# Performance work log

Hardware: AMD Instinct MI355X
Metric: run time of the kernel (lower is better)

## Reference

```python
import jax, jax.numpy as jnp
import numpy as np

N_NODES = 10000
N_EDGES = 320000
D_IN = 256
D_OUT = 256
NEG_SLOPE = 0.2


def setup_inputs() -> dict:
    key = jax.random.key(0)
    ks = jax.random.split(key, 8)
    feature = jax.random.normal(ks[0], (N_NODES, D_IN), dtype=jnp.float32)
    src = jax.random.randint(ks[1], (N_EDGES,), 0, N_NODES, dtype=jnp.int32)
    dst = jax.random.randint(ks[2], (N_EDGES,), 0, N_NODES, dtype=jnp.int32)
    # Xavier-ish scaled weights
    s = 1.0 / np.sqrt(D_IN)
    W_s = jax.random.normal(ks[3], (D_OUT, D_IN), dtype=jnp.float32) * s
    W_t = jax.random.normal(ks[4], (D_OUT, D_IN), dtype=jnp.float32) * s
    W_attn = jax.random.normal(ks[5], (1, D_OUT), dtype=jnp.float32) * (1.0 / np.sqrt(D_OUT))
    W_fc = jax.random.normal(ks[6], (D_OUT, D_IN), dtype=jnp.float32) * s
    b_fc = jnp.zeros((D_OUT,), dtype=jnp.float32)
    return {"feature": feature, "src": src, "dst": dst,
            "W_s": W_s, "W_t": W_t, "W_attn": W_attn,
            "W_fc": W_fc, "b_fc": b_fc}


def reference(feature, src, dst, W_s, W_t, W_attn, W_fc, b_fc):
    n = feature.shape[0]
    # Project at node level, then gather (same math as projecting gathered feats).
    proj_s = feature @ W_s.T          # [N, D_OUT]
    proj_t = feature @ W_t.T          # [N, D_OUT]
    # Edge attention logits: attn(LeakyReLU(h_dst + h_src))
    z = proj_s[src] + proj_t[dst]     # [E, D_OUT]
    z = jnp.where(z >= 0, z, NEG_SLOPE * z)
    e = (z @ W_attn.T)[:, 0]          # [E]
    # edge_softmax with norm_by='src': softmax over outgoing edges of each src node
    m = jax.ops.segment_max(e, src, num_segments=n)          # [N]
    m = jnp.where(jnp.isfinite(m), m, 0.0)                   # guard empty segments
    e_exp = jnp.exp(e - m[src])                               # [E]
    denom = jax.ops.segment_sum(e_exp, src, num_segments=n)  # [N]
    alpha = e_exp / denom[src]                                # [E]
    # message = src feature * alpha; reduce = sum at dst
    msg = feature[src] * alpha[:, None]                       # [E, D_IN]
    agg = jax.ops.segment_sum(msg, dst, num_segments=n)       # [N, D_IN]
    # final linear
    return agg @ W_fc.T + b_fc
```

## Files before the change

### kernel.cpp

```cpp
#include <hip/hip_runtime.h>
#include <math.h>

#define N_NODES 10000
#define N_EDGES 320000
#define D 256
#define NEG_SLOPE 0.2f
#define BCAP 96
#define BLOCK 256
#define NF4 (N_NODES * D / 4)
#define NW4 (256 * 256 / 4)
#define NTILE_M 157
#define NTILES (NTILE_M * 12)
#define FILL_BLOCKS ((N_EDGES + BLOCK - 1) / BLOCK)
#define CPAD 66

typedef unsigned short ushortT;
typedef __attribute__((ext_vector_type(8))) short bf16x8;
typedef __attribute__((ext_vector_type(4))) float f32x4;

__device__ __forceinline__ unsigned short f2bf(float f) {
  unsigned int u = __float_as_uint(f);
  u += 0x7FFFu + ((u >> 16) & 1u);
  return (unsigned short)(u >> 16);
}
__device__ __forceinline__ float bf2f(unsigned short u) {
  return __uint_as_float((unsigned int)u << 16);
}

typedef const __attribute__((address_space(1))) unsigned int* gas_ptr;
typedef __attribute__((address_space(3))) unsigned int* las_ptr;
__device__ __forceinline__ void gload16(const void* g, void* l) {
  __builtin_amdgcn_global_load_lds((gas_ptr)g, (las_ptr)l, 16, 0, 0);
}

__global__ void prep_kernel(const float* __restrict__ feat,
                            const float* __restrict__ Ws,
                            const float* __restrict__ Wt,
                            const float* __restrict__ Wfc,
                            ushortT* __restrict__ featb,
                            ushortT* __restrict__ Wcat,
                            int* __restrict__ cnt,
                            float* __restrict__ denom) {
  const int g = blockIdx.x * blockDim.x + threadIdx.x;
  if (g < NF4) {
    float4 v = ((const float4*)feat)[g];
    ushort4 u;
    u.x = f2bf(v.x); u.y = f2bf(v.y); u.z = f2bf(v.z); u.w = f2bf(v.w);
    ((ushort4*)featb)[g] = u;
    return;
  }
  const int gi = g - NF4;
  if (gi < 3 * NW4) {
    const float* W = (gi < NW4) ? Ws : ((gi < 2 * NW4) ? Wt : Wfc);
    const int off = gi - ((gi < NW4) ? 0 : ((gi < 2 * NW4) ? NW4 : 2 * NW4));
    float4 v = ((const float4*)W)[off];
    ushort4 u;
    u.x = f2bf(v.x); u.y = f2bf(v.y); u.z = f2bf(v.z); u.w = f2bf(v.w);
    ((ushort4*)Wcat)[gi] = u;
    return;
  }
  const int gn = gi - 3 * NW4;
  if (gn < N_NODES) {
    cnt[gn] = 0;
    denom[gn] = 0.f;
  }
}

__global__ __launch_bounds__(256, 2) void proj_fill_kernel(
    const ushortT* __restrict__ featb,
    const ushortT* __restrict__ Wcat,
    const int* __restrict__ src, const int* __restrict__ dst,
    int* __restrict__ cnt, int* __restrict__ src_b,
    ushortT* __restrict__ ps, ushortT* __restrict__ pt,
    ushortT* __restrict__ fcp) {
  __shared__ ushortT Als[64][D];
  __shared__ ushortT Bls[64][D];
  __shared__ ushortT Cls[64][CPAD];

  if (blockIdx.x < FILL_BLOCKS) {
    const int i = blockIdx.x * BLOCK + threadIdx.x;
    if (i < N_EDGES) {
      const int dn = dst[i];
      const int slot = atomicAdd(&cnt[dn], 1);
      if (slot < BCAP) src_b[dn * BCAP + slot] = src[i];
    }
    return;
  }
  const int p = blockIdx.x - FILL_BLOCKS;
  const int m0 = (p / 12) * 64;
  const int by = p % 12;
  ushortT* outp = (by < 4) ? ps : ((by < 8) ? pt : fcp);
  const int col0 = (by & 3) * 64;
  const int n0 = by * 64;

  const int tid = threadIdx.x;
  const int wave = tid >> 6;
  const int lane = tid & 63;
  const int quad = lane >> 4;
  const int l16 = lane & 15;

  const int m_base_t = (wave & 1) * 32;
  const int wn = wave >> 1;

  {
    const int rl = lane >> 5;
    const int cph = lane & 31;
#pragma unroll
    for (int c = 0; c < 8; ++c) {
      const int r = wave * 16 + c * 2 + rl;
      const int clog = cph ^ (r & 7);
      gload16(featb + (size_t)(m0 + r) * D + clog * 8, &Als[wave * 16 + c * 2][0]);
      gload16(Wcat + (size_t)(n0 + r) * D + clog * 8, &Bls[wave * 16 + c * 2][0]);
    }
  }
  __syncthreads();

  f32x4 acc[2][2];
#pragma unroll
  for (int i = 0; i < 2; ++i)
#pragma unroll
    for (int j = 0; j < 2; ++j) acc[i][j] = (f32x4){0.f, 0.f, 0.f, 0.f};

  const int ar0 = m_base_t + l16;
  const int br0 = wn * 32 + l16;
  const int xa = ar0 & 7;
  const int xb = br0 & 7;
#pragma unroll
  for (int kk = 0; kk < 8; ++kk) {
    const int j = kk * 4 + quad;
    const int ea = (j ^ xa) * 8;
    const int eb = (j ^ xb) * 8;
    bf16x8 a0 = *(const bf16x8*)&Als[ar0][ea];
    bf16x8 a1 = *(const bf16x8*)&Als[ar0 + 16][ea];
    bf16x8 b0 = *(const bf16x8*)&Bls[br0][eb];
    bf16x8 b1 = *(const bf16x8*)&Bls[br0 + 16][eb];
    acc[0][0] = __builtin_amdgcn_mfma_f32_16x16x32_bf16(a0, b0, acc[0][0], 0, 0, 0);
    acc[0][1] = __builtin_amdgcn_mfma_f32_16x16x32_bf16(a0, b1, acc[0][1], 0, 0, 0);
    acc[1][0] = __builtin_amdgcn_mfma_f32_16x16x32_bf16(a1, b0, acc[1][0], 0, 0, 0);
    acc[1][1] = __builtin_amdgcn_mfma_f32_16x16x32_bf16(a1, b1, acc[1][1], 0, 0, 0);
  }

#pragma unroll
  for (int mi = 0; mi < 2; ++mi)
#pragma unroll
    for (int r = 0; r < 4; ++r) {
      const int row = m_base_t + mi * 16 + quad * 4 + r;
#pragma unroll
      for (int ni = 0; ni < 2; ++ni)
        Cls[row][wn * 32 + ni * 16 + l16] = f2bf(acc[mi][ni][r]);
    }
  __syncthreads();
#pragma unroll
  for (int it = 0; it < 2; ++it) {
    const int idx = tid + it * 256;
    const int row = idx >> 3;
    const int cc = (idx & 7) * 8;
    const int grow = m0 + row;
    if (grow < N_NODES)
      *(bf16x8*)(outp + (size_t)grow * D + col0 + cc) = *(const bf16x8*)&Cls[row][cc];
  }
}

__global__ __launch_bounds__(256) void logit_bucket_kernel(
    const ushortT* __restrict__ ps,
    const ushortT* __restrict__ pt,
    const int* __restrict__ cnt,
    const int* __restrict__ src_b,
    const float* __restrict__ Wattn,
    float* __restrict__ expv_b,
    float* __restrict__ denom) {
  const int wave = threadIdx.x >> 6;
  const int n = blockIdx.x * 4 + wave;
  if (n >= N_NODES) return;
  const int cn = min(cnt[n], BCAP);
  if (cn == 0) return;
  const int lane = threadIdx.x & 63;
  const int half = lane >> 5;
  const int l32 = lane & 31;
  const int base = n * BCAP;

  bf16x8 bu = *(const bf16x8*)(pt + (size_t)n * D + l32 * 8);
  float b[8], w[8];
  const float4 w0 = *(const float4*)(Wattn + l32 * 8);
  const float4 w1 = *(const float4*)(Wattn + l32 * 8 + 4);
  w[0] = w0.x; w[1] = w0.y; w[2] = w0.z; w[3] = w0.w;
  w[4] = w1.x; w[5] = w1.y; w[6] = w1.z; w[7] = w1.w;
#pragma unroll
  for (int i = 0; i < 8; ++i) b[i] = bf2f((unsigned short)bu[i]);

  int j = half;
  for (; j + 6 < cn; j += 8) {
    const int s0 = src_b[base + j];
    const int s1 = src_b[base + j + 2];
    const int s2 = src_b[base + j + 4];
    const int s3 = src_b[base + j + 6];
    bf16x8 au0 = *(const bf16x8*)(ps + (size_t)s0 * D + l32 * 8);
    bf16x8 au1 = *(const bf16x8*)(ps + (size_t)s1 * D + l32 * 8);
    bf16x8 au2 = *(const bf16x8*)(ps + (size_t)s2 * D + l32 * 8);
    bf16x8 au3 = *(const bf16x8*)(ps + (size_t)s3 * D + l32 * 8);
    float sum0 = 0.f, sum1 = 0.f, sum2 = 0.f, sum3 = 0.f;
#pragma unroll
    for (int i = 0; i < 8; ++i) {
      float z0 = bf2f((unsigned short)au0[i]) + b[i];
      float z1 = bf2f((unsigned short)au1[i]) + b[i];
      float z2 = bf2f((unsigned short)au2[i]) + b[i];
      float z3 = bf2f((unsigned short)au3[i]) + b[i];
      z0 = fmaxf(z0, NEG_SLOPE * z0);
      z1 = fmaxf(z1, NEG_SLOPE * z1);
      z2 = fmaxf(z2, NEG_SLOPE * z2);
      z3 = fmaxf(z3, NEG_SLOPE * z3);
      sum0 = fmaf(w[i], z0, sum0);
      sum1 = fmaf(w[i], z1, sum1);
      sum2 = fmaf(w[i], z2, sum2);
      sum3 = fmaf(w[i], z3, sum3);
    }
#pragma unroll
    for (int off = 16; off > 0; off >>= 1) {
      sum0 += __shfl_down(sum0, off, 32);
      sum1 += __shfl_down(sum1, off, 32);
      sum2 += __shfl_down(sum2, off, 32);
      sum3 += __shfl_down(sum3, off, 32);
    }
    if (l32 == 0) {
      float ex0 = __expf(sum0), ex1 = __expf(sum1);
      float ex2 = __expf(sum2), ex3 = __expf(sum3);
      expv_b[base + j] = ex0;
      expv_b[base + j + 2] = ex1;
      expv_b[base + j + 4] = ex2;
      expv_b[base + j + 6] = ex3;
      atomicAdd(&denom[s0], ex0);
      atomicAdd(&denom[s1], ex1);
      atomicAdd(&denom[s2], ex2);
      atomicAdd(&denom[s3], ex3);
    }
  }
  for (; j < cn; j += 2) {
    const int s = src_b[base + j];
    bf16x8 au = *(const bf16x8*)(ps + (size_t)s * D + l32 * 8);
    float sum = 0.f;
#pragma unroll
    for (int i = 0; i < 8; ++i) {
      float z = bf2f((unsigned short)au[i]) + b[i];
      z = fmaxf(z, NEG_SLOPE * z);
      sum = fmaf(w[i], z, sum);
    }
#pragma unroll
    for (int off = 16; off > 0; off >>= 1) sum += __shfl_down(sum, off, 32);
    if (l32 == 0) {
      float ex = __expf(sum);
      expv_b[base + j] = ex;
      atomicAdd(&denom[s], ex);
    }
  }
}

__global__ __launch_bounds__(256) void gather_agg_kernel(
    const ushortT* __restrict__ fcp,
    const int* __restrict__ cnt,
    const int* __restrict__ src_b,
    const float* __restrict__ expv_b,
    const float* __restrict__ denom,
    const float* __restrict__ b_fc,
    float* __restrict__ out) {
  const int wave = threadIdx.x >> 6;
  const int n = blockIdx.x * 4 + wave;
  if (n >= N_NODES) return;
  const int lane = threadIdx.x & 63;
  const int half = lane >> 5;
  const int l32 = lane & 31;
  const int cn = min(cnt[n], BCAP);
  const int base = n * BCAP;

  float acc[8];
#pragma unroll
  for (int i = 0; i < 8; ++i) acc[i] = 0.f;

  int j = half;
  for (; j + 6 < cn; j += 8) {
    const int s0 = src_b[base + j];
    const int s1 = src_b[base + j + 2];
    const int s2 = src_b[base + j + 4];
    const int s3 = src_b[base + j + 6];
    const float a0 = expv_b[base + j] / denom[s0];
    const float a1 = expv_b[base + j + 2] / denom[s1];
    const float a2 = expv_b[base + j + 4] / denom[s2];
    const float a3 = expv_b[base + j + 6] / denom[s3];
    bf16x8 f0 = *(const bf16x8*)(fcp + (size_t)s0 * D + l32 * 8);
    bf16x8 f1 = *(const bf16x8*)(fcp + (size_t)s1 * D + l32 * 8);
    bf16x8 f2 = *(const bf16x8*)(fcp + (size_t)s2 * D + l32 * 8);
    bf16x8 f3 = *(const bf16x8*)(fcp + (size_t)s3 * D + l32 * 8);
#pragma unroll
    for (int i = 0; i < 8; ++i) {
      acc[i] = fmaf(a0, bf2f((unsigned short)f0[i]), acc[i]);
      acc[i] = fmaf(a1, bf2f((unsigned short)f1[i]), acc[i]);
      acc[i] = fmaf(a2, bf2f((unsigned short)f2[i]), acc[i]);
      acc[i] = fmaf(a3, bf2f((unsigned short)f3[i]), acc[i]);
    }
  }
  for (; j < cn; j += 2) {
    const int s = src_b[base + j];
    const float a = expv_b[base + j] / denom[s];
    bf16x8 fu = *(const bf16x8*)(fcp + (size_t)s * D + l32 * 8);
#pragma unroll
    for (int i = 0; i < 8; ++i)
      acc[i] = fmaf(a, bf2f((unsigned short)fu[i]), acc[i]);
  }
#pragma unroll
  for (int i = 0; i < 8; ++i) acc[i] += __shfl_xor(acc[i], 32);
  if (half == 0) {
    const float4 bf0 = *(const float4*)(b_fc + l32 * 8);
    const float4 bf1 = *(const float4*)(b_fc + l32 * 8 + 4);
    float4 o0 = make_float4(acc[0] + bf0.x, acc[1] + bf0.y, acc[2] + bf0.z, acc[3] + bf0.w);
    float4 o1 = make_float4(acc[4] + bf1.x, acc[5] + bf1.y, acc[6] + bf1.z, acc[7] + bf1.w);
    *(float4*)(out + (size_t)n * D + l32 * 8) = o0;
    *(float4*)(out + (size_t)n * D + l32 * 8 + 4) = o1;
  }
}

extern "C" void kernel_launch(void* const* d_in, const int* in_sizes, int n_in,
                              void* d_out, int out_size, void* d_ws, size_t ws_size,
                              hipStream_t stream) {
  const float* feat  = (const float*)d_in[0];
  const int*   src   = (const int*)d_in[1];
  const int*   dst   = (const int*)d_in[2];
  const float* Ws    = (const float*)d_in[3];
  const float* Wt    = (const float*)d_in[4];
  const float* Wattn = (const float*)d_in[5];
  const float* Wfc   = (const float*)d_in[6];
  const float* bfc   = (const float*)d_in[7];
  float* out = (float*)d_out;

  ushortT* ps    = (ushortT*)d_ws;
  ushortT* pt    = ps + (size_t)N_NODES * D;
  ushortT* fcp   = pt + (size_t)N_NODES * D;
  ushortT* featb = fcp + (size_t)N_NODES * D;
  ushortT* Wcat  = featb + (size_t)N_NODES * D;
  float* expv_b  = (float*)(Wcat + (size_t)768 * 256);
  float* denom   = expv_b + (size_t)N_NODES * BCAP;
  int*   cnt     = (int*)(denom + N_NODES);
  int*   src_b   = cnt + N_NODES;

  const int prep_items = NF4 + 3 * NW4 + N_NODES;
  const int nodeblocks = (N_NODES + 3) / 4;
  prep_kernel<<<(prep_items + BLOCK - 1) / BLOCK, BLOCK, 0, stream>>>(
      feat, Ws, Wt, Wfc, featb, Wcat, cnt, denom);
  proj_fill_kernel<<<FILL_BLOCKS + NTILES, BLOCK, 0, stream>>>(
      featb, Wcat, src, dst, cnt, src_b, ps, pt, fcp);
  logit_bucket_kernel<<<nodeblocks, BLOCK, 0, stream>>>(ps, pt, cnt, src_b, Wattn, expv_b, denom);
  gather_agg_kernel<<<nodeblocks, BLOCK, 0, stream>>>(fcp, cnt, src_b, expv_b, denom, bfc, out);
}
```

Before: 162.1 us.

## Load B tile into registers, vectorize edge index loads, use fast reciprocal

The projection GEMM now loads its weight fragments straight from global memory into registers instead of staging them in LDS. That removes the Bls buffer, and the occupancy hint rises from 2 to 3 blocks. The attention and aggregate kernels now have each half-wave handle four contiguous edge slots, read with int4/float4 vector loads and written with a float4 store, instead of strided scalar accesses. The exact division by denom is replaced with a v_rcp_f32 reciprocal times the value, trading a little precision for fewer instructions. The extra register arrays may raise register pressure against the higher occupancy target.

```diff
diff --git a/kernel.cpp b/kernel.cpp
--- a/kernel.cpp
+++ b/kernel.cpp
@@ -25,6 +25,11 @@
 }
 __device__ __forceinline__ float bf2f(unsigned short u) {
   return __uint_as_float((unsigned int)u << 16);
+}
+__device__ __forceinline__ float fastrcp(float x) {
+  float r;
+  asm volatile("v_rcp_f32 %0, %1" : "=v"(r) : "v"(x));
+  return r;
 }
 
 typedef const __attribute__((address_space(1))) unsigned int* gas_ptr;
@@ -66,7 +71,7 @@
   }
 }
 
-__global__ __launch_bounds__(256, 2) void proj_fill_kernel(
+__global__ __launch_bounds__(256, 3) void proj_fill_kernel(
     const ushortT* __restrict__ featb,
     const ushortT* __restrict__ Wcat,
     const int* __restrict__ src, const int* __restrict__ dst,
@@ -74,7 +79,6 @@
     ushortT* __restrict__ ps, ushortT* __restrict__ pt,
     ushortT* __restrict__ fcp) {
   __shared__ ushortT Als[64][D];
-  __shared__ ushortT Bls[64][D];
   __shared__ ushortT Cls[64][CPAD];
 
   if (blockIdx.x < FILL_BLOCKS) {
@@ -101,6 +105,14 @@
 
   const int m_base_t = (wave & 1) * 32;
   const int wn = wave >> 1;
+  const int br0 = wn * 32 + l16;
+
+  bf16x8 b0r[8], b1r[8];
+#pragma unroll
+  for (int kk = 0; kk < 8; ++kk) {
+    b0r[kk] = *(const bf16x8*)(Wcat + (size_t)(n0 + br0) * D + kk * 32 + quad * 8);
+    b1r[kk] = *(const bf16x8*)(Wcat + (size_t)(n0 + br0 + 16) * D + kk * 32 + quad * 8);
+  }
 
   {
     const int rl = lane >> 5;
@@ -110,7 +122,6 @@
       const int r = wave * 16 + c * 2 + rl;
       const int clog = cph ^ (r & 7);
       gload16(featb + (size_t)(m0 + r) * D + clog * 8, &Als[wave * 16 + c * 2][0]);
-      gload16(Wcat + (size_t)(n0 + r) * D + clog * 8, &Bls[wave * 16 + c * 2][0]);
     }
   }
   __syncthreads();
@@ -122,22 +133,16 @@
     for (int j = 0; j < 2; ++j) acc[i][j] = (f32x4){0.f, 0.f, 0.f, 0.f};
 
   const int ar0 = m_base_t + l16;
-  const int br0 = wn * 32 + l16;
   const int xa = ar0 & 7;
-  const int xb = br0 & 7;
 #pragma unroll
   for (int kk = 0; kk < 8; ++kk) {
-    const int j = kk * 4 + quad;
-    const int ea = (j ^ xa) * 8;
-    const int eb = (j ^ xb) * 8;
+    const int ea = ((kk * 4 + quad) ^ xa) * 8;
     bf16x8 a0 = *(const bf16x8*)&Als[ar0][ea];
     bf16x8 a1 = *(const bf16x8*)&Als[ar0 + 16][ea];
-    bf16x8 b0 = *(const bf16x8*)&Bls[br0][eb];
-    bf16x8 b1 = *(const bf16x8*)&Bls[br0 + 16][eb];
-    acc[0][0] = __builtin_amdgcn_mfma_f32_16x16x32_bf16(a0, b0, acc[0][0], 0, 0, 0);
-    acc[0][1] = __builtin_amdgcn_mfma_f32_16x16x32_bf16(a0, b1, acc[0][1], 0, 0, 0);
-    acc[1][0] = __builtin_amdgcn_mfma_f32_16x16x32_bf16(a1, b0, acc[1][0], 0, 0, 0);
-    acc[1][1] = __builtin_amdgcn_mfma_f32_16x16x32_bf16(a1, b1, acc[1][1], 0, 0, 0);
+    acc[0][0] = __builtin_amdgcn_mfma_f32_16x16x32_bf16(a0, b0r[kk], acc[0][0], 0, 0, 0);
+    acc[0][1] = __builtin_amdgcn_mfma_f32_16x16x32_bf16(a0, b1r[kk], acc[0][1], 0, 0, 0);
+    acc[1][0] = __builtin_amdgcn_mfma_f32_16x16x32_bf16(a1, b0r[kk], acc[1][0], 0, 0, 0);
+    acc[1][1] = __builtin_amdgcn_mfma_f32_16x16x32_bf16(a1, b1r[kk], acc[1][1], 0, 0, 0);
   }
 
 #pragma unroll
@@ -188,16 +193,13 @@
 #pragma unroll
   for (int i = 0; i < 8; ++i) b[i] = bf2f((unsigned short)bu[i]);
 
-  int j = half;
-  for (; j + 6 < cn; j += 8) {
-    const int s0 = src_b[base + j];
-    const int s1 = src_b[base + j + 2];
-    const int s2 = src_b[base + j + 4];
-    const int s3 = src_b[base + j + 6];
-    bf16x8 au0 = *(const bf16x8*)(ps + (size_t)s0 * D + l32 * 8);
-    bf16x8 au1 = *(const bf16x8*)(ps + (size_t)s1 * D + l32 * 8);
-    bf16x8 au2 = *(const bf16x8*)(ps + (size_t)s2 * D + l32 * 8);
-    bf16x8 au3 = *(const bf16x8*)(ps + (size_t)s3 * D + l32 * 8);
+  const int cn4 = cn & ~7;
+  for (int j = half * 4; j < cn4; j += 8) {
+    const int4 s4 = *(const int4*)(src_b + base + j);
+    bf16x8 au0 = *(const bf16x8*)(ps + (size_t)s4.x * D + l32 * 8);
+    bf16x8 au1 = *(const bf16x8*)(ps + (size_t)s4.y * D + l32 * 8);
+    bf16x8 au2 = *(const bf16x8*)(ps + (size_t)s4.z * D + l32 * 8);
+    bf16x8 au3 = *(const bf16x8*)(ps + (size_t)s4.w * D + l32 * 8);
     float sum0 = 0.f, sum1 = 0.f, sum2 = 0.f, sum3 = 0.f;
 #pragma unroll
     for (int i = 0; i < 8; ++i) {
@@ -224,17 +226,14 @@
     if (l32 == 0) {
       float ex0 = __expf(sum0), ex1 = __expf(sum1);
       float ex2 = __expf(sum2), ex3 = __expf(sum3);
-      expv_b[base + j] = ex0;
-      expv_b[base + j + 2] = ex1;
-      expv_b[base + j + 4] = ex2;
-      expv_b[base + j + 6] = ex3;
-      atomicAdd(&denom[s0], ex0);
-      atomicAdd(&denom[s1], ex1);
-      atomicAdd(&denom[s2], ex2);
-      atomicAdd(&denom[s3], ex3);
-    }
-  }
-  for (; j < cn; j += 2) {
+      *(float4*)(expv_b + base + j) = make_float4(ex0, ex1, ex2, ex3);
+      atomicAdd(&denom[s4.x], ex0);
+      atomicAdd(&denom[s4.y], ex1);
+      atomicAdd(&denom[s4.z], ex2);
+      atomicAdd(&denom[s4.w], ex3);
+    }
+  }
+  for (int j = cn4 + half; j < cn; j += 2) {
     const int s = src_b[base + j];
     bf16x8 au = *(const bf16x8*)(ps + (size_t)s * D + l32 * 8);
     float sum = 0.f;
@@ -275,20 +274,18 @@
 #pragma unroll
   for (int i = 0; i < 8; ++i) acc[i] = 0.f;
 
-  int j = half;
-  for (; j + 6 < cn; j += 8) {
-    const int s0 = src_b[base + j];
-    const int s1 = src_b[base + j + 2];
-    const int s2 = src_b[base + j + 4];
-    const int s3 = src_b[base + j + 6];
-    const float a0 = expv_b[base + j] / denom[s0];
-    const float a1 = expv_b[base + j + 2] / denom[s1];
-    const float a2 = expv_b[base + j + 4] / denom[s2];
-    const float a3 = expv_b[base + j + 6] / denom[s3];
-    bf16x8 f0 = *(const bf16x8*)(fcp + (size_t)s0 * D + l32 * 8);
-    bf16x8 f1 = *(const bf16x8*)(fcp + (size_t)s1 * D + l32 * 8);
-    bf16x8 f2 = *(const bf16x8*)(fcp + (size_t)s2 * D + l32 * 8);
-    bf16x8 f3 = *(const bf16x8*)(fcp + (size_t)s3 * D + l32 * 8);
+  const int cn4 = cn & ~7;
+  for (int j = half * 4; j < cn4; j += 8) {
+    const int4 s4 = *(const int4*)(src_b + base + j);
+    const float4 e4 = *(const float4*)(expv_b + base + j);
+    const float a0 = e4.x * fastrcp(denom[s4.x]);
+    const float a1 = e4.y * fastrcp(denom[s4.y]);
+    const float a2 = e4.z * fastrcp(denom[s4.z]);
+    const float a3 = e4.w * fastrcp(denom[s4.w]);
+    bf16x8 f0 = *(const bf16x8*)(fcp + (size_t)s4.x * D + l32 * 8);
+    bf16x8 f1 = *(const bf16x8*)(fcp + (size_t)s4.y * D + l32 * 8);
+    bf16x8 f2 = *(const bf16x8*)(fcp + (size_t)s4.z * D + l32 * 8);
+    bf16x8 f3 = *(const bf16x8*)(fcp + (size_t)s4.w * D + l32 * 8);
 #pragma unroll
     for (int i = 0; i < 8; ++i) {
       acc[i] = fmaf(a0, bf2f((unsigned short)f0[i]), acc[i]);
@@ -297,9 +294,9 @@
       acc[i] = fmaf(a3, bf2f((unsigned short)f3[i]), acc[i]);
     }
   }
-  for (; j < cn; j += 2) {
+  for (int j = cn4 + half; j < cn; j += 2) {
     const int s = src_b[base + j];
-    const float a = expv_b[base + j] / denom[s];
+    const float a = expv_b[base + j] * fastrcp(denom[s]);
     bf16x8 fu = *(const bf16x8*)(fcp + (size_t)s * D + l32 * 8);
 #pragma unroll
     for (int i = 0; i < 8; ++i)
```

Result: slower. 175.3 us (+8.1%).
